# Performance work log

Hardware: AMD Instinct MI355X
Metric: run time of the kernel (lower is better)

## Reference

```python
import jax, jax.numpy as jnp
import numpy as np

B, CIN, CE, CA, N, S = 2, 64, 128, 128, 1024, 32
SCALE = np.sqrt(np.float32(CA))  # scale_mode == 'dimfts'


def _vnlin(W, x):
    # VNLinear: linear map over the channel dim of (B, C, 3, N, S)
    return jnp.einsum('oc,bcdns->bodns', W, x)


def setup_inputs() -> dict:
    key = jax.random.key(0)
    ks = jax.random.split(key, 16)
    def w(k, o, i):
        return (jax.random.normal(k, (o, i), jnp.float32) / np.sqrt(np.float32(i)))
    return {
        'group_xyz': jax.random.normal(ks[0], (B, N, S, 3), jnp.float32),
        'group_fts': jax.random.normal(ks[1], (B, CIN, 3, N, S), jnp.float32),
        'query_xyz': jax.random.normal(ks[2], (B, N, 3), jnp.float32),
        'W_e1': w(ks[3], CE, CIN), 'W_e2': w(ks[4], CE, CE),
        'W_q': w(ks[5], CA, CE), 'W_k': w(ks[6], CA, CE), 'W_v': w(ks[7], CA, CE),
        'W_r1': w(ks[8], 64, 1), 'W_r2': w(ks[9], CA, 64),
        'W_std': w(ks[10], 3, CA),
        'W_f1': w(ks[11], CA, CA * 3), 'b_f1': jax.random.normal(ks[12], (CA,), jnp.float32) * 0.02,
        'W_f2': w(ks[13], CA, CA), 'b_f2': jax.random.normal(ks[14], (CA,), jnp.float32) * 0.02,
    }


def reference(group_xyz, group_fts, query_xyz, W_e1, W_e2, W_q, W_k, W_v,
              W_r1, W_r2, W_std, W_f1, b_f1, W_f2, b_f2):
    # vnn_e: two stacked VNLinear layers
    group_emb = _vnlin(W_e2, _vnlin(W_e1, group_fts))        # (B, CE, 3, N, S)
    query_emb = group_emb[..., :1]                           # (B, CE, 3, N, 1)
    q = _vnlin(W_q, query_emb)                               # (B, CA, 3, N, 1)
    k = _vnlin(W_k, group_emb)                               # (B, CA, 3, N, S)
    v = _vnlin(W_v, group_emb)                               # (B, CA, 3, N, S)

    # positional relation: xyz_rel -> (B, 1, 3, N, S) -> vnn_r
    xyz_rel = group_xyz - query_xyz[:, :, None, :]           # (B, N, S, 3)
    xyz_rel = jnp.transpose(xyz_rel[:, :, :, None, :], (0, 3, 4, 1, 2))  # (B,1,3,N,S)
    pos_rel = _vnlin(W_r2, _vnlin(W_r1, xyz_rel))            # (B, CA, 3, N, S)

    # relation_func == 'sub'
    attn = q - k + pos_rel                                   # (B, CA, 3, N, S)

    # VNStdFeatureLin (dim=5, no frame normalization): z0 = VNLinear(CA->3)
    z0 = _vnlin(W_std, attn)                                 # (B, 3, 3, N, S)
    attn = jnp.einsum('bijns,bjkns->bikns', attn, z0)        # (B, CA, 3, N, S) invariant

    # attn_fwd: 1x1 conv -> ReLU -> 1x1 conv on (B, CA*3, N, S)
    attn = attn.reshape(B, CA * 3, N, S)
    h = jax.nn.relu(jnp.einsum('oc,bcns->bons', W_f1, attn) + b_f1[:, None, None])
    a = jnp.einsum('oc,bcns->bons', W_f2, h) + b_f2[:, None, None]  # (B, CA, N, S)

    a = jax.nn.softmax(a[:, :, None, :, :] / SCALE, axis=-1)  # (B, CA, 1, N, S)
    v = v + pos_rel
    resi = jnp.sum(a * v, axis=-1)                            # (B, CA, 3, N)
    return resi
```

## Files before the change

### kernel.cpp

```cpp
#include <hip/hip_runtime.h>
#include <hip/hip_bf16.h>
#include <math.h>

typedef __hip_bfloat16  bf16;
typedef __hip_bfloat162 bf162;
typedef __attribute__((ext_vector_type(8))) short short8;
typedef __attribute__((ext_vector_type(4))) float f32x4;

#define BB   2
#define CINC 64
#define NN   1024
#define SSS  32
#define NS   (NN * SSS)

#define OFF_WE21 0
#define OFF_WR   8192
#define OFF_KBA  8320
#define OFF_VB   16512
#define OFF_F1B  20608
#define OFF_F2B  45184
#define WS_NEED_FLOATS 53376

#define S_ATT_B  0
#define S_FTS_B  26112
#define S_SCR_B  26112
#define S_XYZ_B  30720
#define SMEM_BYTES 30912

__device__ __forceinline__ float bf2f(short s) {
    unsigned int u = ((unsigned int)(unsigned short)s) << 16;
    return __uint_as_float(u);
}
__device__ __forceinline__ short f2bf(float f) {
    bf16 h = __float2bfloat16(f);
    return *reinterpret_cast<short*>(&h);
}
__device__ __forceinline__ unsigned pk2(float a, float b) {
    bf162 p = __float22bfloat162_rn(make_float2(a, b));
    return *reinterpret_cast<unsigned*>(&p);
}

__global__ __launch_bounds__(256) void prep1(const float* __restrict__ We1,
                                             const float* __restrict__ We2,
                                             float* __restrict__ ws) {
    int e = blockIdx.x * 256 + threadIdx.x;
    int o = e >> 6, c = e & 63;
    float acc = 0.f;
    for (int m = 0; m < 128; ++m)
        acc = fmaf(We2[o * 128 + m], We1[m * 64 + c], acc);
    ws[OFF_WE21 + o * 64 + c] = acc;
}

__global__ __launch_bounds__(256) void prep2(const float* __restrict__ Wq,
                                             const float* __restrict__ Wk,
                                             const float* __restrict__ Wv,
                                             const float* __restrict__ Wr1,
                                             const float* __restrict__ Wr2,
                                             const float* __restrict__ Wf1,
                                             const float* __restrict__ Wf2,
                                             float* __restrict__ ws) {
    const float* we21 = ws + OFF_WE21;
    int e = blockIdx.x * 256 + threadIdx.x;
    if (e < 16384) {
        int i = e >> 7, c2 = e & 127;
        const float* W = (c2 < 64) ? Wk : Wq;
        int c = c2 & 63;
        float acc = 0.f;
        for (int o = 0; o < 128; ++o)
            acc = fmaf(W[i * 128 + o], we21[o * 64 + c], acc);
        if (c2 >= 64) acc = -acc;
        ((bf16*)(ws + OFF_KBA))[i * 128 + c2] = __float2bfloat16(acc);
    } else if (e < 24576) {
        int le = e - 16384;
        int i = le >> 6, c = le & 63;
        float acc = 0.f;
        for (int o = 0; o < 128; ++o)
            acc = fmaf(Wv[i * 128 + o], we21[o * 64 + c], acc);
        ((bf16*)(ws + OFF_VB))[i * 64 + c] = __float2bfloat16(acc);
    } else if (e < 24704) {
        int i = e - 24576;
        float acc = 0.f;
        for (int m = 0; m < 64; ++m)
            acc = fmaf(Wr2[i * 64 + m], Wr1[m], acc);
        ws[OFF_WR + i] = acc;
    } else if (e < 24704 + 49152) {
        int f = e - 24704;
        int o = f / 384, kp = f - o * 384;
        int c = (kp & 127) * 3 + (kp >> 7);
        ((bf16*)(ws + OFF_F1B))[f] = __float2bfloat16(Wf1[o * 384 + c]);
    } else if (e < 24704 + 49152 + 16384) {
        int f = e - (24704 + 49152);
        ((bf16*)(ws + OFF_F2B))[f] = __float2bfloat16(Wf2[f]);
    }
}

__global__ __launch_bounds__(256, 4) void fused_main(
        const float* __restrict__ gxyz, const float* __restrict__ gfts,
        const float* __restrict__ qxyz, const float* __restrict__ Wstd,
        const float* __restrict__ bf1,  const float* __restrict__ bf2,
        const float* __restrict__ ws,   float* __restrict__ out) {
    extern __shared__ char smc[];
    short* s_att  = (short*)(smc + S_ATT_B);
    short* h_t    = s_att;
    short* a_t    = s_att + 4352;
    short* fts_s  = (short*)(smc + S_FTS_B);
    float* s_scr  = (float*)(smc + S_SCR_B);
    short* s_xyzh = (short*)(smc + S_XYZ_B);

    const int t    = threadIdx.x;
    const int bid  = blockIdx.x;
    const int b    = bid >> 10;
    const int n    = bid & 1023;
    const int w    = t >> 6;
    const int lane = t & 63;
    const int quad = lane >> 4;
    const int lq   = lane & 15;
    const int wb   = 32 * w;

    const float* gb = gfts + (size_t)b * (CINC * 3 * NS) + n * SSS;
    const short* kba = (const short*)(ws + OFF_KBA);

    short8 Ka[2][2], Va[2][2];
    {
        const short* vbb = (const short*)(ws + OFF_VB);
        #pragma unroll
        for (int it = 0; it < 2; ++it) {
            int i = wb + it * 16 + lq;
            #pragma unroll
            for (int kc = 0; kc < 2; ++kc)
                Ka[it][kc] = *(const short8*)(kba + i * 128 + kc * 32 + quad * 8);
            #pragma unroll
            for (int kc = 0; kc < 2; ++kc)
                Va[it][kc] = *(const short8*)(vbb + i * 64 + kc * 32 + quad * 8);
        }
    }
    float wr2[2] = { ws[OFF_WR + wb + lq], ws[OFF_WR + wb + 16 + lq] };

    uint2 va_pk[6][2];
    #pragma unroll
    for (int h = 0; h < 3; ++h) {
        {
            int cp = t >> 3;
            int ml = (t & 7) * 4;
            const float* fb = gb + (2 * cp * 3 + h) * NS + ml;
            float4 f0 = *(const float4*)(fb);
            float4 f1 = *(const float4*)(fb + 3 * NS);
            short* dst = fts_s + ml * 72 + 2 * cp;
            *(unsigned*)(dst)       = pk2(f0.x, f1.x);
            *(unsigned*)(dst + 72)  = pk2(f0.y, f1.y);
            *(unsigned*)(dst + 144) = pk2(f0.z, f1.z);
            *(unsigned*)(dst + 216) = pk2(f0.w, f1.w);
        }
        if (h == 0 && t >= 160) {
            int id = t - 160;
            int d = id >> 5, s = id & 31;
            s_xyzh[id] = f2bf(gxyz[((b * NN + n) * SSS + s) * 3 + d]
                              - qxyz[(b * NN + n) * 3 + d]);
        }
        __syncthreads();

        float qv[2];
        {
            const short* qp = fts_s + quad * 8;
            short8 aq0 = *(const short8*)(qp);
            short8 aq1 = *(const short8*)(qp + 32);
            #pragma unroll
            for (int it = 0; it < 2; ++it) {
                int i = wb + it * 16 + lq;
                short8 kq2 = *(const short8*)(kba + i * 128 + 64 + quad * 8);
                short8 kq3 = *(const short8*)(kba + i * 128 + 96 + quad * 8);
                f32x4 qa = {0.f, 0.f, 0.f, 0.f};
                qa = __builtin_amdgcn_mfma_f32_16x16x32_bf16(aq0, kq2, qa, 0, 0, 0);
                qa = __builtin_amdgcn_mfma_f32_16x16x32_bf16(aq1, kq3, qa, 0, 0, 0);
                qv[it] = qa[0];
            }
        }
        #pragma unroll
        for (int mt_h = 0; mt_h < 2; ++mt_h) {
            int mt = h * 2 + mt_h;
            const short* ap = fts_s + (mt_h * 16 + lq) * 72 + quad * 8;
            short8 a0 = *(const short8*)(ap);
            short8 a1 = *(const short8*)(ap + 32);
            #pragma unroll
            for (int it = 0; it < 2; ++it) {
                f32x4 kk = {0.f, 0.f, 0.f, 0.f};
                kk = __builtin_amdgcn_mfma_f32_16x16x32_bf16(a0, Ka[it][0], kk, 0, 0, 0);
                kk = __builtin_amdgcn_mfma_f32_16x16x32_bf16(a1, Ka[it][1], kk, 0, 0, 0);
                f32x4 vv = {0.f, 0.f, 0.f, 0.f};
                vv = __builtin_amdgcn_mfma_f32_16x16x32_bf16(a0, Va[it][0], vv, 0, 0, 0);
                vv = __builtin_amdgcn_mfma_f32_16x16x32_bf16(a1, Va[it][1], vv, 0, 0, 0);
                int i = wb + it * 16 + lq;
                float p[4];
                #pragma unroll
                for (int reg = 0; reg < 4; ++reg) {
                    int m = mt * 16 + quad * 4 + reg;
                    float pos = wr2[it] * bf2f(s_xyzh[m]);
                    s_att[m * 136 + i] = f2bf(pos - kk[reg] - qv[it]);
                    p[reg] = vv[reg] + pos;
                }
                va_pk[mt][it].x = pk2(p[0], p[1]);
                va_pk[mt][it].y = pk2(p[2], p[3]);
            }
        }
        __syncthreads();
    }

    {
        short8 As[4];
        #pragma unroll
        for (int kc = 0; kc < 4; ++kc) {
            short8 a = {0, 0, 0, 0, 0, 0, 0, 0};
            if (lq < 3) {
                const float* wp = Wstd + lq * 128 + kc * 32 + quad * 8;
                float4 w0 = *(const float4*)(wp);
                float4 w1 = *(const float4*)(wp + 4);
                a[0] = f2bf(w0.x); a[1] = f2bf(w0.y); a[2] = f2bf(w0.z); a[3] = f2bf(w0.w);
                a[4] = f2bf(w1.x); a[5] = f2bf(w1.y); a[6] = f2bf(w1.z); a[7] = f2bf(w1.w);
            }
            As[kc] = a;
        }
        for (int tile = w; tile < 6; tile += 4) {
            f32x4 acc = {0.f, 0.f, 0.f, 0.f};
            const short* bp = s_att + (tile * 16 + lq) * 136 + quad * 8;
            #pragma unroll
            for (int kc = 0; kc < 4; ++kc) {
                short8 bfr = *(const short8*)(bp + kc * 32);
                acc = __builtin_amdgcn_mfma_f32_16x16x32_bf16(As[kc], bfr, acc, 0, 0, 0);
            }
            if (quad == 0) {
                #pragma unroll
                for (int reg = 0; reg < 3; ++reg)
                    s_scr[reg * 96 + tile * 16 + lq] = acc[reg];
            }
        }
    }
    __syncthreads();

    for (int u = t; u < 512; u += 256) {
        int s  = u >> 4;
        int i0 = (u & 15) * 8;
        float z[3][3];
        #pragma unroll
        for (int j = 0; j < 3; ++j)
            #pragma unroll
            for (int kk = 0; kk < 3; ++kk)
                z[j][kk] = s_scr[j * 96 + kk * 32 + s];
        float af[3][8];
        #pragma unroll
        for (int j = 0; j < 3; ++j) {
            short8 v8 = *(const short8*)(s_att + (j * 32 + s) * 136 + i0);
            #pragma unroll
            for (int x = 0; x < 8; ++x) af[j][x] = bf2f(v8[x]);
        }
        #pragma unroll
        for (int kk = 0; kk < 3; ++kk) {
            short8 o8;
            #pragma unroll
            for (int x = 0; x < 8; ++x)
                o8[x] = f2bf(af[0][x] * z[0][kk] + af[1][x] * z[1][kk] + af[2][x] * z[2][kk]);
            *(short8*)(s_att + (kk * 32 + s) * 136 + i0) = o8;
        }
    }
    __syncthreads();

    f32x4 eacc[2][2];
    {
        f32x4 zz = {0.f, 0.f, 0.f, 0.f};
        eacc[0][0] = zz; eacc[0][1] = zz; eacc[1][0] = zz; eacc[1][1] = zz;
        const short* f1b = (const short*)(ws + OFF_F1B);
        const short* ab0 = f1b + (wb + lq) * 384 + quad * 8;
        const short* ab1 = ab0 + 16 * 384;
        #pragma unroll 2
        for (int ks = 0; ks < 12; ++ks) {
            int kk = ks >> 2;
            int ic = (ks & 3) * 32 + quad * 8;
            short8 a0 = *(const short8*)(ab0 + ks * 32);
            short8 a1 = *(const short8*)(ab1 + ks * 32);
            const short* bp = s_att + (kk * 32) * 136 + ic;
            short8 b0 = *(const short8*)(bp + lq * 136);
            short8 b1 = *(const short8*)(bp + (lq + 16) * 136);
            eacc[0][0] = __builtin_amdgcn_mfma_f32_16x16x32_bf16(a0, b0, eacc[0][0], 0, 0, 0);
            eacc[0][1] = __builtin_amdgcn_mfma_f32_16x16x32_bf16(a0, b1, eacc[0][1], 0, 0, 0);
            eacc[1][0] = __builtin_amdgcn_mfma_f32_16x16x32_bf16(a1, b0, eacc[1][0], 0, 0, 0);
            eacc[1][1] = __builtin_amdgcn_mfma_f32_16x16x32_bf16(a1, b1, eacc[1][1], 0, 0, 0);
        }
    }
    __syncthreads();

    #pragma unroll
    for (int mt = 0; mt < 2; ++mt) {
        int ob = wb + mt * 16 + quad * 4;
        float4 bb = *(const float4*)(bf1 + ob);
        float bv[4] = {bb.x, bb.y, bb.z, bb.w};
        #pragma unroll
        for (int nt = 0; nt < 2; ++nt) {
            f32x4 c = eacc[mt][nt];
            int s = nt * 16 + lq;
            uint2 pk;
            pk.x = pk2(fmaxf(c[0] + bv[0], 0.f), fmaxf(c[1] + bv[1], 0.f));
            pk.y = pk2(fmaxf(c[2] + bv[2], 0.f), fmaxf(c[3] + bv[3], 0.f));
            *(uint2*)(h_t + s * 136 + ob) = pk;
        }
    }
    __syncthreads();

    {
        f32x4 facc[2][2];
        f32x4 zz = {0.f, 0.f, 0.f, 0.f};
        facc[0][0] = zz; facc[0][1] = zz; facc[1][0] = zz; facc[1][1] = zz;
        const short* f2b = (const short*)(ws + OFF_F2B);
        const short* ab0 = f2b + (wb + lq) * 128 + quad * 8;
        const short* ab1 = ab0 + 16 * 128;
        #pragma unroll 2
        for (int ks = 0; ks < 4; ++ks) {
            int c0 = ks * 32 + quad * 8;
            short8 a0 = *(const short8*)(ab0 + ks * 32);
            short8 a1 = *(const short8*)(ab1 + ks * 32);
            short8 b0 = *(const short8*)(h_t + lq * 136 + c0);
            short8 b1 = *(const short8*)(h_t + (lq + 16) * 136 + c0);
            facc[0][0] = __builtin_amdgcn_mfma_f32_16x16x32_bf16(a0, b0, facc[0][0], 0, 0, 0);
            facc[0][1] = __builtin_amdgcn_mfma_f32_16x16x32_bf16(a0, b1, facc[0][1], 0, 0, 0);
            facc[1][0] = __builtin_amdgcn_mfma_f32_16x16x32_bf16(a1, b0, facc[1][0], 0, 0, 0);
            facc[1][1] = __builtin_amdgcn_mfma_f32_16x16x32_bf16(a1, b1, facc[1][1], 0, 0, 0);
        }
        const float inv = 0.08838834764831845f;
        #pragma unroll
        for (int mt = 0; mt < 2; ++mt) {
            int ob = wb + mt * 16 + quad * 4;
            float4 bb = *(const float4*)(bf2 + ob);
            float bv[4] = {bb.x, bb.y, bb.z, bb.w};
            float a0v[4], a1v[4];
            #pragma unroll
            for (int reg = 0; reg < 4; ++reg) {
                float v0 = facc[mt][0][reg] + bv[reg];
                float v1 = facc[mt][1][reg] + bv[reg];
                float mx = fmaxf(v0, v1);
                mx = fmaxf(mx, __shfl_xor(mx, 1));
                mx = fmaxf(mx, __shfl_xor(mx, 2));
                mx = fmaxf(mx, __shfl_xor(mx, 4));
                mx = fmaxf(mx, __shfl_xor(mx, 8));
                float e0 = __expf((v0 - mx) * inv);
                float e1 = __expf((v1 - mx) * inv);
                float sm = e0 + e1;
                sm += __shfl_xor(sm, 1);
                sm += __shfl_xor(sm, 2);
                sm += __shfl_xor(sm, 4);
                sm += __shfl_xor(sm, 8);
                float rs = 1.f / sm;
                a0v[reg] = e0 * rs;
                a1v[reg] = e1 * rs;
            }
            uint2 pk;
            pk.x = pk2(a0v[0], a0v[1]);
            pk.y = pk2(a0v[2], a0v[3]);
            *(uint2*)(a_t + lq * 136 + ob) = pk;
            pk.x = pk2(a1v[0], a1v[1]);
            pk.y = pk2(a1v[2], a1v[3]);
            *(uint2*)(a_t + (16 + lq) * 136 + ob) = pk;
        }
    }
    __syncthreads();

    {
        float pr[2][3];
        #pragma unroll
        for (int it = 0; it < 2; ++it)
            #pragma unroll
            for (int d = 0; d < 3; ++d) pr[it][d] = 0.f;
        #pragma unroll
        for (int mt = 0; mt < 6; ++mt) {
            int d = mt >> 1;
            int s0 = (mt & 1) * 16 + quad * 4;
            #pragma unroll
            for (int it = 0; it < 2; ++it) {
                int i = wb + it * 16 + lq;
                uint2 vp = va_pk[mt][it];
                float v0 = bf2f((short)(vp.x & 0xffff));
                float v1 = bf2f((short)(vp.x >> 16));
                float v2 = bf2f((short)(vp.y & 0xffff));
                float v3 = bf2f((short)(vp.y >> 16));
                pr[it][d] = fmaf(bf2f(a_t[(s0 + 0) * 136 + i]), v0, pr[it][d]);
                pr[it][d] = fmaf(bf2f(a_t[(s0 + 1) * 136 + i]), v1, pr[it][d]);
                pr[it][d] = fmaf(bf2f(a_t[(s0 + 2) * 136 + i]), v2, pr[it][d]);
                pr[it][d] = fmaf(bf2f(a_t[(s0 + 3) * 136 + i]), v3, pr[it][d]);
            }
        }
        #pragma unroll
        for (int it = 0; it < 2; ++it)
            #pragma unroll
            for (int d = 0; d < 3; ++d) {
                float v = pr[it][d];
                v += __shfl_xor(v, 16);
                v += __shfl_xor(v, 32);
                if (quad == 0) s_scr[(wb + it * 16 + lq) * 3 + d] = v;
            }
    }
    __syncthreads();

    for (int e = t; e < 384; e += 256)
        out[(b * 384 + e) * NN + n] = s_scr[e];
}

extern "C" void kernel_launch(void* const* d_in, const int* in_sizes, int n_in,
                              void* d_out, int out_size, void* d_ws, size_t ws_size,
                              hipStream_t stream) {
    const float* gxyz = (const float*)d_in[0];
    const float* gfts = (const float*)d_in[1];
    const float* qxyz = (const float*)d_in[2];
    const float* We1  = (const float*)d_in[3];
    const float* We2  = (const float*)d_in[4];
    const float* Wq   = (const float*)d_in[5];
    const float* Wk   = (const float*)d_in[6];
    const float* Wv   = (const float*)d_in[7];
    const float* Wr1  = (const float*)d_in[8];
    const float* Wr2  = (const float*)d_in[9];
    const float* Wstd = (const float*)d_in[10];
    const float* bf1  = (const float*)d_in[12];
    const float* bf2  = (const float*)d_in[14];
    float* out = (float*)d_out;
    float* ws  = (float*)d_ws;

    (void)hipFuncSetAttribute((const void*)fused_main,
                              hipFuncAttributeMaxDynamicSharedMemorySize, SMEM_BYTES);

    prep1<<<32, 256, 0, stream>>>(We1, We2, ws);
    prep2<<<353, 256, 0, stream>>>(Wq, Wk, Wv, Wr1, Wr2,
                                   (const float*)d_in[11], (const float*)d_in[13], ws);
    fused_main<<<BB * NN, 256, SMEM_BYTES, stream>>>(gxyz, gfts, qxyz, Wstd,
                                                     bf1, bf2, ws, out);
}
```

Before: 199.7 us.

## Defer V projection to the final reduction to cut register pressure

```diff
diff --git a/kernel.cpp b/kernel.cpp
--- a/kernel.cpp
+++ b/kernel.cpp
@@ -23,9 +23,8 @@
 
 #define S_ATT_B  0
 #define S_FTS_B  26112
-#define S_SCR_B  26112
-#define S_XYZ_B  30720
-#define SMEM_BYTES 30912
+#define S_XYZ_B  39936
+#define SMEM_BYTES 40128
 
 __device__ __forceinline__ float bf2f(short s) {
     unsigned int u = ((unsigned int)(unsigned short)s) << 16;
@@ -104,8 +103,8 @@
     short* h_t    = s_att;
     short* a_t    = s_att + 4352;
     short* fts_s  = (short*)(smc + S_FTS_B);
-    float* s_scr  = (float*)(smc + S_SCR_B);
     short* s_xyzh = (short*)(smc + S_XYZ_B);
+    float* s_red  = (float*)(smc + S_ATT_B);
 
     const int t    = threadIdx.x;
     const int bid  = blockIdx.x;
@@ -120,23 +119,16 @@
     const float* gb = gfts + (size_t)b * (CINC * 3 * NS) + n * SSS;
     const short* kba = (const short*)(ws + OFF_KBA);
 
-    short8 Ka[2][2], Va[2][2];
-    {
-        const short* vbb = (const short*)(ws + OFF_VB);
-        #pragma unroll
-        for (int it = 0; it < 2; ++it) {
-            int i = wb + it * 16 + lq;
-            #pragma unroll
-            for (int kc = 0; kc < 2; ++kc)
-                Ka[it][kc] = *(const short8*)(kba + i * 128 + kc * 32 + quad * 8);
-            #pragma unroll
-            for (int kc = 0; kc < 2; ++kc)
-                Va[it][kc] = *(const short8*)(vbb + i * 64 + kc * 32 + quad * 8);
-        }
+    short8 Ka[2][2];
+    #pragma unroll
+    for (int it = 0; it < 2; ++it) {
+        int i = wb + it * 16 + lq;
+        #pragma unroll
+        for (int kc = 0; kc < 2; ++kc)
+            Ka[it][kc] = *(const short8*)(kba + i * 128 + kc * 32 + quad * 8);
     }
     float wr2[2] = { ws[OFF_WR + wb + lq], ws[OFF_WR + wb + 16 + lq] };
 
-    uint2 va_pk[6][2];
     #pragma unroll
     for (int h = 0; h < 3; ++h) {
         {
@@ -145,7 +137,7 @@
             const float* fb = gb + (2 * cp * 3 + h) * NS + ml;
             float4 f0 = *(const float4*)(fb);
             float4 f1 = *(const float4*)(fb + 3 * NS);
-            short* dst = fts_s + ml * 72 + 2 * cp;
+            short* dst = fts_s + (h * 32 + ml) * 72 + 2 * cp;
             *(unsigned*)(dst)       = pk2(f0.x, f1.x);
             *(unsigned*)(dst + 72)  = pk2(f0.y, f1.y);
             *(unsigned*)(dst + 144) = pk2(f0.z, f1.z);
@@ -161,7 +153,7 @@
 
         float qv[2];
         {
-            const short* qp = fts_s + quad * 8;
+            const short* qp = fts_s + (h * 32) * 72 + quad * 8;
             short8 aq0 = *(const short8*)(qp);
             short8 aq1 = *(const short8*)(qp + 32);
             #pragma unroll
@@ -178,7 +170,7 @@
         #pragma unroll
         for (int mt_h = 0; mt_h < 2; ++mt_h) {
             int mt = h * 2 + mt_h;
-            const short* ap = fts_s + (mt_h * 16 + lq) * 72 + quad * 8;
+            const short* ap = fts_s + (h * 32 + mt_h * 16 + lq) * 72 + quad * 8;
             short8 a0 = *(const short8*)(ap);
             short8 a1 = *(const short8*)(ap + 32);
             #pragma unroll
@@ -186,20 +178,13 @@
                 f32x4 kk = {0.f, 0.f, 0.f, 0.f};
                 kk = __builtin_amdgcn_mfma_f32_16x16x32_bf16(a0, Ka[it][0], kk, 0, 0, 0);
                 kk = __builtin_amdgcn_mfma_f32_16x16x32_bf16(a1, Ka[it][1], kk, 0, 0, 0);
-                f32x4 vv = {0.f, 0.f, 0.f, 0.f};
-                vv = __builtin_amdgcn_mfma_f32_16x16x32_bf16(a0, Va[it][0], vv, 0, 0, 0);
-                vv = __builtin_amdgcn_mfma_f32_16x16x32_bf16(a1, Va[it][1], vv, 0, 0, 0);
                 int i = wb + it * 16 + lq;
-                float p[4];
                 #pragma unroll
                 for (int reg = 0; reg < 4; ++reg) {
                     int m = mt * 16 + quad * 4 + reg;
                     float pos = wr2[it] * bf2f(s_xyzh[m]);
                     s_att[m * 136 + i] = f2bf(pos - kk[reg] - qv[it]);
-                    p[reg] = vv[reg] + pos;
                 }
-                va_pk[mt][it].x = pk2(p[0], p[1]);
-                va_pk[mt][it].y = pk2(p[2], p[3]);
             }
         }
         __syncthreads();
@@ -228,9 +213,10 @@
                 acc = __builtin_amdgcn_mfma_f32_16x16x32_bf16(As[kc], bfr, acc, 0, 0, 0);
             }
             if (quad == 0) {
+                float* hp = (float*)(fts_s + (tile * 16 + lq) * 72 + 64);
                 #pragma unroll
                 for (int reg = 0; reg < 3; ++reg)
-                    s_scr[reg * 96 + tile * 16 + lq] = acc[reg];
+                    hp[reg] = acc[reg];
             }
         }
     }
@@ -241,10 +227,12 @@
         int i0 = (u & 15) * 8;
         float z[3][3];
         #pragma unroll
-        for (int j = 0; j < 3; ++j)
-            #pragma unroll
-            for (int kk = 0; kk < 3; ++kk)
-                z[j][kk] = s_scr[j * 96 + kk * 32 + s];
+        for (int kk = 0; kk < 3; ++kk) {
+            const float* hp = (const float*)(fts_s + (kk * 32 + s) * 72 + 64);
+            #pragma unroll
+            for (int j = 0; j < 3; ++j)
+                z[j][kk] = hp[j];
+        }
         float af[3][8];
         #pragma unroll
         for (int j = 0; j < 3; ++j) {
@@ -362,27 +350,42 @@
     __syncthreads();
 
     {
-        float pr[2][3];
-        #pragma unroll
-        for (int it = 0; it < 2; ++it)
-            #pragma unroll
-            for (int d = 0; d < 3; ++d) pr[it][d] = 0.f;
-        #pragma unroll
-        for (int mt = 0; mt < 6; ++mt) {
-            int d = mt >> 1;
-            int s0 = (mt & 1) * 16 + quad * 4;
+        __builtin_amdgcn_sched_barrier(0);
+        short8 Va[2][2];
+        {
+            const short* vbb = (const short*)(ws + OFF_VB);
             #pragma unroll
             for (int it = 0; it < 2; ++it) {
                 int i = wb + it * 16 + lq;
-                uint2 vp = va_pk[mt][it];
-                float v0 = bf2f((short)(vp.x & 0xffff));
-                float v1 = bf2f((short)(vp.x >> 16));
-                float v2 = bf2f((short)(vp.y & 0xffff));
-                float v3 = bf2f((short)(vp.y >> 16));
-                pr[it][d] = fmaf(bf2f(a_t[(s0 + 0) * 136 + i]), v0, pr[it][d]);
-                pr[it][d] = fmaf(bf2f(a_t[(s0 + 1) * 136 + i]), v1, pr[it][d]);
-                pr[it][d] = fmaf(bf2f(a_t[(s0 + 2) * 136 + i]), v2, pr[it][d]);
-                pr[it][d] = fmaf(bf2f(a_t[(s0 + 3) * 136 + i]), v3, pr[it][d]);
+                #pragma unroll
+                for (int kc = 0; kc < 2; ++kc)
+                    Va[it][kc] = *(const short8*)(vbb + i * 64 + kc * 32 + quad * 8);
+            }
+        }
+        float pr[2][3];
+        #pragma unroll
+        for (int it = 0; it < 2; ++it)
+            #pragma unroll
+            for (int d = 0; d < 3; ++d) pr[it][d] = 0.f;
+        #pragma unroll
+        for (int mt = 0; mt < 6; ++mt) {
+            int d  = mt >> 1;
+            int s0 = (mt & 1) * 16 + quad * 4;
+            const short* ap = fts_s + (mt * 16 + lq) * 72 + quad * 8;
+            short8 a0 = *(const short8*)(ap);
+            short8 a1 = *(const short8*)(ap + 32);
+            #pragma unroll
+            for (int it = 0; it < 2; ++it) {
+                f32x4 vv = {0.f, 0.f, 0.f, 0.f};
+                vv = __builtin_amdgcn_mfma_f32_16x16x32_bf16(a0, Va[it][0], vv, 0, 0, 0);
+                vv = __builtin_amdgcn_mfma_f32_16x16x32_bf16(a1, Va[it][1], vv, 0, 0, 0);
+                int i = wb + it * 16 + lq;
+                #pragma unroll
+                for (int reg = 0; reg < 4; ++reg) {
+                    int m = mt * 16 + quad * 4 + reg;
+                    float vp = vv[reg] + wr2[it] * bf2f(s_xyzh[m]);
+                    pr[it][d] = fmaf(bf2f(a_t[(s0 + reg) * 136 + i]), vp, pr[it][d]);
+                }
             }
         }
         #pragma unroll
@@ -392,13 +395,13 @@
                 float v = pr[it][d];
                 v += __shfl_xor(v, 16);
                 v += __shfl_xor(v, 32);
-                if (quad == 0) s_scr[(wb + it * 16 + lq) * 3 + d] = v;
+                if (quad == 0) s_red[(wb + it * 16 + lq) * 3 + d] = v;
             }
     }
     __syncthreads();
 
     for (int e = t; e < 384; e += 256)
-        out[(b * 384 + e) * NN + n] = s_scr[e];
+        out[(b * 384 + e) * NN + n] = s_red[e];
 }
 
 extern "C" void kernel_launch(void* const* d_in, const int* in_sizes, int n_in,
```

Result: faster. 177.8 us (-11.0%).
